# Optimization experiments

Measured on AMD Instinct MI355X. Metric: run time of the kernel, lower is better.

The kernel has to match this reference:

```python
import jax, jax.numpy as jnp
import numpy as np

MARGIN = 0.3


def setup_inputs() -> dict:
    key = jax.random.key(0)
    k1, k2 = jax.random.split(key)
    B, D = 4096, 1024
    z_anchor = jax.random.normal(k1, (B, D), dtype=jnp.float32)
    z_positive = jax.random.normal(k2, (B, D), dtype=jnp.float32)
    return {"z_anchor": z_anchor, "z_positive": z_positive}


def reference(z_anchor, z_positive):
    B = z_anchor.shape[0]
    a = z_anchor / jnp.linalg.norm(z_anchor, axis=1, keepdims=True)
    p = z_positive / jnp.linalg.norm(z_positive, axis=1, keepdims=True)

    pos_dist = 1.0 - jnp.sum(a * p, axis=1)                 # [B]
    neg_dist_mat = 1.0 - jnp.einsum('bd,cd->bc', a, p)      # [B,B]

    offdiag = ~jnp.eye(B, dtype=bool)
    pd = pos_dist[:, None]
    semi_hard = offdiag & (neg_dist_mat > pd) & (neg_dist_mat < pd + MARGIN)

    cnt = jnp.sum(semi_hard, axis=1)                        # [B]
    mean_semi = jnp.sum(jnp.where(semi_hard, neg_dist_mat, 0.0), axis=1) / jnp.maximum(cnt, 1)
    min_offdiag = jnp.min(jnp.where(offdiag, neg_dist_mat, jnp.inf), axis=1)

    neg_dist = jnp.where(cnt > 0, mean_semi, min_offdiag)   # [B]
    loss = jnp.mean(jax.nn.relu(pos_dist - neg_dist + MARGIN))
    return loss
```

## Files before the change

### kernel.cpp

```cpp
#include <hip/hip_runtime.h>
#include <stdint.h>

#define MARGIN 0.3f

typedef __bf16 bf16x8_t __attribute__((ext_vector_type(8)));
typedef float f32x4_t __attribute__((ext_vector_type(4)));

static constexpr int NB = 4096;
static constexpr int ND = 1024;
static constexpr int NKT = ND / 64;
static constexpr int NIT = NKT / 2;

__device__ __forceinline__ unsigned short f2bf(float x) {
  union { float f; unsigned u; } v; v.f = x;
  unsigned r = v.u + 0x7FFFu + ((v.u >> 16) & 1u);
  return (unsigned short)(r >> 16);
}

__device__ __forceinline__ void gload_lds16(const void* g, void* l) {
  __builtin_amdgcn_global_load_lds(
      reinterpret_cast<const __attribute__((address_space(1))) uint32_t*>(
          reinterpret_cast<uintptr_t>(g)),
      reinterpret_cast<__attribute__((address_space(3))) uint32_t*>(
          reinterpret_cast<uintptr_t>(l)),
      16, 0, 0);
}

__global__ __launch_bounds__(256) void norm_kernel(
    const float* __restrict__ za, const float* __restrict__ zp,
    __bf16* __restrict__ Ah, __bf16* __restrict__ Ph,
    float* __restrict__ pos, float* __restrict__ ssum,
    int* __restrict__ scnt, unsigned* __restrict__ smin) {
  const int b = blockIdx.x;
  const int t = threadIdx.x;
  const float4 av = reinterpret_cast<const float4*>(za + (size_t)b * ND)[t];
  const float4 pv = reinterpret_cast<const float4*>(zp + (size_t)b * ND)[t];
  float sa = av.x * av.x + av.y * av.y + av.z * av.z + av.w * av.w;
  float sp = pv.x * pv.x + pv.y * pv.y + pv.z * pv.z + pv.w * pv.w;
  float dp = av.x * pv.x + av.y * pv.y + av.z * pv.z + av.w * pv.w;
#pragma unroll
  for (int off = 1; off < 64; off <<= 1) {
    sa += __shfl_xor(sa, off);
    sp += __shfl_xor(sp, off);
    dp += __shfl_xor(dp, off);
  }
  __shared__ float red[3][4];
  const int wid = t >> 6, lane = t & 63;
  if (lane == 0) { red[0][wid] = sa; red[1][wid] = sp; red[2][wid] = dp; }
  __syncthreads();
  sa = red[0][0] + red[0][1] + red[0][2] + red[0][3];
  sp = red[1][0] + red[1][1] + red[1][2] + red[1][3];
  dp = red[2][0] + red[2][1] + red[2][2] + red[2][3];
  const float rsa = rsqrtf(sa), rsp = rsqrtf(sp);
  if (t == 0) {
    pos[b] = 1.0f - dp * rsa * rsp;
    ssum[b] = 0.0f;
    scnt[b] = 0;
    smin[b] = 0x7F800000u;
  }
  ushort4 oa, op;
  oa.x = f2bf(av.x * rsa); oa.y = f2bf(av.y * rsa);
  oa.z = f2bf(av.z * rsa); oa.w = f2bf(av.w * rsa);
  op.x = f2bf(pv.x * rsp); op.y = f2bf(pv.y * rsp);
  op.z = f2bf(pv.z * rsp); op.w = f2bf(pv.w * rsp);
  reinterpret_cast<ushort4*>(reinterpret_cast<unsigned short*>(Ah) + (size_t)b * ND)[t] = oa;
  reinterpret_cast<ushort4*>(reinterpret_cast<unsigned short*>(Ph) + (size_t)b * ND)[t] = op;
}


#define BAR   __builtin_amdgcn_s_barrier()
#define LGKM0 asm volatile("s_waitcnt lgkmcnt(0)" ::: "memory")
#define VM4   asm volatile("s_waitcnt vmcnt(4)" ::: "memory")
#define VM0   asm volatile("s_waitcnt vmcnt(0)" ::: "memory")
#define PRIO1 __builtin_amdgcn_s_setprio(1)
#define PRIO0 __builtin_amdgcn_s_setprio(0)

#define STAGE_A(buf, half, kt) do { \
    const char* _g = (const char*)Ah + (size_t)(row0 + (half)*128 + srow) * 2048 + (size_t)(kt)*128 + scolb; \
    char* _l = smem + (buf)*32768 + (half)*16384 + w*1024; \
    gload_lds16(_g, _l); \
    gload_lds16(_g + 64*2048, _l + 8192); \
  } while (0)

#define STAGE_B(buf, half, kt) do { \
    const char* _g = (const char*)Ph + (size_t)(col0 + (half)*128 + srow) * 2048 + (size_t)(kt)*128 + scolb; \
    char* _l = smem + 65536 + (buf)*32768 + (half)*16384 + w*1024; \
    gload_lds16(_g, _l); \
    gload_lds16(_g + 64*2048, _l + 8192); \
  } while (0)

#define LD_A(buf, mh) do { _Pragma("unroll") \
    for (int mm = 0; mm < 4; ++mm) { \
      const char* _p = smem + (buf)*32768 + (wr*128 + (mh)*64 + mm*16 + c) * 128; \
      aq[mm][0] = *(const bf16x8_t*)(_p + cswz0); \
      aq[mm][1] = *(const bf16x8_t*)(_p + cswz1); \
    } } while (0)

#define LD_B(buf, nh, dst) do { _Pragma("unroll") \
    for (int nn = 0; nn < 2; ++nn) { \
      const char* _p = smem + 65536 + (buf)*32768 + (wc*64 + (nh)*32 + nn*16 + c) * 128; \
      dst[nn][0] = *(const bf16x8_t*)(_p + cswz0); \
      dst[nn][1] = *(const bf16x8_t*)(_p + cswz1); \
    } } while (0)

#define MFMA_Q(mh, bq, nh) do { _Pragma("unroll") \
    for (int kk = 0; kk < 2; ++kk) { _Pragma("unroll") \
      for (int mm = 0; mm < 4; ++mm) { _Pragma("unroll") \
        for (int nn = 0; nn < 2; ++nn) \
          acc[(mh)*4+mm][(nh)*2+nn] = __builtin_amdgcn_mfma_f32_16x16x32_bf16( \
              aq[mm][kk], bq[nn][kk], acc[(mh)*4+mm][(nh)*2+nn], 0, 0, 0); \
      } } } while (0)

__global__ __launch_bounds__(512, 2) void gemm8_kernel(
    const __bf16* __restrict__ Ah, const __bf16* __restrict__ Ph,
    const float* __restrict__ pos, float* __restrict__ ssum,
    int* __restrict__ scnt, unsigned* __restrict__ smin) {
  extern __shared__ char smem[];
  const int t = threadIdx.x;
  const int lane = t & 63;
  const int w = t >> 6;
  const int wr = w >> 2, wc = w & 3;
  const int c = lane & 15, g = lane >> 4;

  const int wg = blockIdx.x;
  const int swzid = (wg & 7) * 32 + (wg >> 3);
  const int by = swzid >> 4, bx = swzid & 15;
  const int row0 = by * 256, col0 = bx * 256;

  const int srow = w * 8 + (lane >> 3);
  const int scolb = ((lane & 7) << 4) ^ (((lane >> 3) & 7) << 4);
  const int cswz0 = (g * 16) ^ ((c & 7) << 4);
  const int cswz1 = (64 + g * 16) ^ ((c & 7) << 4);

  f32x4_t acc[8][4] = {};
  bf16x8_t aq[4][2], bq0[2][2], bq1[2][2];

  STAGE_B(0, 0, 0); STAGE_B(0, 1, 0);
  STAGE_A(0, 0, 0); STAGE_A(0, 1, 0);
  STAGE_B(1, 0, 1); STAGE_B(1, 1, 1);
  VM4; BAR;

  for (int i = 0; i < NIT; ++i) {
    const int o = 2 * i + 1;
    const bool st = (i < NIT - 1);
    LD_A(0, 0); LD_B(0, 0, bq0);
    STAGE_A(1, 0, o);
    BAR; LGKM0; PRIO1; MFMA_Q(0, bq0, 0); PRIO0; BAR;
    LD_B(0, 1, bq1);
    STAGE_A(1, 1, o);
    BAR; LGKM0; PRIO1; MFMA_Q(0, bq1, 1); PRIO0; BAR;
    LD_A(0, 1);
    if (st) STAGE_B(0, 0, o + 1);
    BAR; LGKM0; PRIO1; MFMA_Q(1, bq0, 0); PRIO0; BAR;
    if (st) STAGE_B(0, 1, o + 1);
    PRIO1; MFMA_Q(1, bq1, 1); PRIO0;
    if (st) { VM4; } else { VM0; }
    BAR;
    LD_A(1, 0); LD_B(1, 0, bq0);
    if (st) STAGE_A(0, 0, o + 1);
    BAR; LGKM0; PRIO1; MFMA_Q(0, bq0, 0); PRIO0; BAR;
    LD_B(1, 1, bq1);
    if (st) STAGE_A(0, 1, o + 1);
    BAR; LGKM0; PRIO1; MFMA_Q(0, bq1, 1); PRIO0; BAR;
    LD_A(1, 1);
    if (st) STAGE_B(1, 0, o + 2);
    BAR; LGKM0; PRIO1; MFMA_Q(1, bq0, 0); PRIO0; BAR;
    if (st) STAGE_B(1, 1, o + 2);
    PRIO1; MFMA_Q(1, bq1, 1); PRIO0;
    if (st) { VM4; } else { VM0; }
    BAR;
  }

#pragma unroll
  for (int m = 0; m < 8; ++m) {
#pragma unroll
    for (int r = 0; r < 4; ++r) {
      const int grow = row0 + wr * 128 + m * 16 + g * 4 + r;
      const float pd = pos[grow];
      float s = 0.0f;
      int ct = 0;
      float mn = 3.0e38f;
#pragma unroll
      for (int n = 0; n < 4; ++n) {
        const int gcol = col0 + wc * 64 + n * 16 + c;
        const float v = 1.0f - acc[m][n][r];
        if (gcol != grow) {
          mn = fminf(mn, v);
          if (v > pd && v < pd + MARGIN) { s += v; ct += 1; }
        }
      }
#pragma unroll
      for (int off = 1; off < 16; off <<= 1) {
        s += __shfl_xor(s, off);
        ct += __shfl_xor(ct, off);
        mn = fminf(mn, __shfl_xor(mn, off));
      }
      if (c == 0) {
        atomicAdd(&ssum[grow], s);
        atomicAdd(&scnt[grow], ct);
        atomicMin(&smin[grow], __float_as_uint(mn));
      }
    }
  }
}

__global__ __launch_bounds__(256) void finalize_kernel(
    const float* __restrict__ pos, const float* __restrict__ ssum,
    const int* __restrict__ scnt, const unsigned* __restrict__ smin,
    float* __restrict__ out) {
  const int t = threadIdx.x;
  float accv = 0.0f;
#pragma unroll
  for (int it = 0; it < NB / 256; ++it) {
    const int rr = t + it * 256;
    const float pd = pos[rr];
    const int ct = scnt[rr];
    const float neg = ct > 0 ? ssum[rr] / (float)ct : __uint_as_float(smin[rr]);
    accv += fmaxf(pd - neg + MARGIN, 0.0f);
  }
#pragma unroll
  for (int off = 1; off < 64; off <<= 1) accv += __shfl_xor(accv, off);
  __shared__ float red[4];
  if ((t & 63) == 0) red[t >> 6] = accv;
  __syncthreads();
  if (t == 0) out[0] = (red[0] + red[1] + red[2] + red[3]) * (1.0f / NB);
}

extern "C" void kernel_launch(void* const* d_in, const int* in_sizes, int n_in,
                              void* d_out, int out_size, void* d_ws, size_t ws_size,
                              hipStream_t stream) {
  const float* za = (const float*)d_in[0];
  const float* zp = (const float*)d_in[1];
  float* out = (float*)d_out;
  char* ws = (char*)d_ws;
  __bf16* Ah = (__bf16*)(ws);
  __bf16* Ph = (__bf16*)(ws + (size_t)NB * ND * 2);
  float* pos = (float*)(ws + (size_t)NB * ND * 4);
  float* ssum = pos + NB;
  int* scnt = (int*)(ssum + NB);
  unsigned* smin = (unsigned*)(scnt + NB);

  (void)hipFuncSetAttribute((const void*)gemm8_kernel,
                            hipFuncAttributeMaxDynamicSharedMemorySize, 131072);

  norm_kernel<<<NB, 256, 0, stream>>>(za, zp, Ah, Ph, pos, ssum, scnt, smin);
  gemm8_kernel<<<256, 512, 131072, stream>>>(Ah, Ph, pos, ssum, scnt, smin);
  finalize_kernel<<<1, 256, 0, stream>>>(pos, ssum, scnt, smin, out);
}
```

Before: 133.8 us.

## Restructure GEMM pipeline with double A register banks and fuse finalize via last-block

```diff
diff --git a/kernel.cpp b/kernel.cpp
--- a/kernel.cpp
+++ b/kernel.cpp
@@ -10,6 +10,7 @@
 static constexpr int ND = 1024;
 static constexpr int NKT = ND / 64;
 static constexpr int NIT = NKT / 2;
+static constexpr int GRID = 256;
 
 __device__ __forceinline__ unsigned short f2bf(float x) {
   union { float f; unsigned u; } v; v.f = x;
@@ -30,7 +31,8 @@
     const float* __restrict__ za, const float* __restrict__ zp,
     __bf16* __restrict__ Ah, __bf16* __restrict__ Ph,
     float* __restrict__ pos, float* __restrict__ ssum,
-    int* __restrict__ scnt, unsigned* __restrict__ smin) {
+    int* __restrict__ scnt, unsigned* __restrict__ smin,
+    int* __restrict__ done) {
   const int b = blockIdx.x;
   const int t = threadIdx.x;
   const float4 av = reinterpret_cast<const float4*>(za + (size_t)b * ND)[t];
@@ -57,6 +59,7 @@
     ssum[b] = 0.0f;
     scnt[b] = 0;
     smin[b] = 0x7F800000u;
+    if (b == 0) *done = 0;
   }
   ushort4 oa, op;
   oa.x = f2bf(av.x * rsa); oa.y = f2bf(av.y * rsa);
@@ -69,9 +72,9 @@
 
 
 #define BAR   __builtin_amdgcn_s_barrier()
-#define LGKM0 asm volatile("s_waitcnt lgkmcnt(0)" ::: "memory")
-#define VM4   asm volatile("s_waitcnt vmcnt(4)" ::: "memory")
-#define VM0   asm volatile("s_waitcnt vmcnt(0)" ::: "memory")
+#define SB0   __builtin_amdgcn_sched_barrier(0)
+#define VM4S  do { asm volatile("s_waitcnt vmcnt(4)" ::: "memory"); SB0; } while (0)
+#define VM0S  do { asm volatile("s_waitcnt vmcnt(0)" ::: "memory"); SB0; } while (0)
 #define PRIO1 __builtin_amdgcn_s_setprio(1)
 #define PRIO0 __builtin_amdgcn_s_setprio(0)
 
@@ -89,32 +92,33 @@
     gload_lds16(_g + 64*2048, _l + 8192); \
   } while (0)
 
-#define LD_A(buf, mh) do { _Pragma("unroll") \
+#define LD_An(buf, mh, bank) do { _Pragma("unroll") \
     for (int mm = 0; mm < 4; ++mm) { \
       const char* _p = smem + (buf)*32768 + (wr*128 + (mh)*64 + mm*16 + c) * 128; \
-      aq[mm][0] = *(const bf16x8_t*)(_p + cswz0); \
-      aq[mm][1] = *(const bf16x8_t*)(_p + cswz1); \
+      bank[mm][0] = *(const bf16x8_t*)(_p + cswz0); \
+      bank[mm][1] = *(const bf16x8_t*)(_p + cswz1); \
     } } while (0)
 
-#define LD_B(buf, nh, dst) do { _Pragma("unroll") \
+#define LD_Bn(buf, nh) do { _Pragma("unroll") \
     for (int nn = 0; nn < 2; ++nn) { \
       const char* _p = smem + 65536 + (buf)*32768 + (wc*64 + (nh)*32 + nn*16 + c) * 128; \
-      dst[nn][0] = *(const bf16x8_t*)(_p + cswz0); \
-      dst[nn][1] = *(const bf16x8_t*)(_p + cswz1); \
+      bq[nn][0] = *(const bf16x8_t*)(_p + cswz0); \
+      bq[nn][1] = *(const bf16x8_t*)(_p + cswz1); \
     } } while (0)
 
-#define MFMA_Q(mh, bq, nh) do { _Pragma("unroll") \
+#define MFMA_Q(mh, nh, ab) do { _Pragma("unroll") \
     for (int kk = 0; kk < 2; ++kk) { _Pragma("unroll") \
       for (int mm = 0; mm < 4; ++mm) { _Pragma("unroll") \
         for (int nn = 0; nn < 2; ++nn) \
           acc[(mh)*4+mm][(nh)*2+nn] = __builtin_amdgcn_mfma_f32_16x16x32_bf16( \
-              aq[mm][kk], bq[nn][kk], acc[(mh)*4+mm][(nh)*2+nn], 0, 0, 0); \
+              ab[mm][kk], bq[nn][kk], acc[(mh)*4+mm][(nh)*2+nn], 0, 0, 0); \
       } } } while (0)
 
 __global__ __launch_bounds__(512, 2) void gemm8_kernel(
     const __bf16* __restrict__ Ah, const __bf16* __restrict__ Ph,
     const float* __restrict__ pos, float* __restrict__ ssum,
-    int* __restrict__ scnt, unsigned* __restrict__ smin) {
+    int* __restrict__ scnt, unsigned* __restrict__ smin,
+    int* __restrict__ done, float* __restrict__ out) {
   extern __shared__ char smem[];
   const int t = threadIdx.x;
   const int lane = t & 63;
@@ -133,42 +137,52 @@
   const int cswz1 = (64 + g * 16) ^ ((c & 7) << 4);
 
   f32x4_t acc[8][4] = {};
-  bf16x8_t aq[4][2], bq0[2][2], bq1[2][2];
-
+  bf16x8_t aqX[4][2], aqY[4][2], bq[2][2];
+
+  STAGE_A(0, 0, 0); STAGE_A(0, 1, 0);
   STAGE_B(0, 0, 0); STAGE_B(0, 1, 0);
-  STAGE_A(0, 0, 0); STAGE_A(0, 1, 0);
-  STAGE_B(1, 0, 1); STAGE_B(1, 1, 1);
-  VM4; BAR;
-
-  for (int i = 0; i < NIT; ++i) {
+  STAGE_A(1, 0, 1); STAGE_A(1, 1, 1);
+  VM4S;
+  BAR;
+  LD_An(0, 0, aqX);
+
+  for (int i = 0; i < NIT - 1; ++i) {
     const int o = 2 * i + 1;
-    const bool st = (i < NIT - 1);
-    LD_A(0, 0); LD_B(0, 0, bq0);
-    STAGE_A(1, 0, o);
-    BAR; LGKM0; PRIO1; MFMA_Q(0, bq0, 0); PRIO0; BAR;
-    LD_B(0, 1, bq1);
-    STAGE_A(1, 1, o);
-    BAR; LGKM0; PRIO1; MFMA_Q(0, bq1, 1); PRIO0; BAR;
-    LD_A(0, 1);
-    if (st) STAGE_B(0, 0, o + 1);
-    BAR; LGKM0; PRIO1; MFMA_Q(1, bq0, 0); PRIO0; BAR;
-    if (st) STAGE_B(0, 1, o + 1);
-    PRIO1; MFMA_Q(1, bq1, 1); PRIO0;
-    if (st) { VM4; } else { VM0; }
-    BAR;
-    LD_A(1, 0); LD_B(1, 0, bq0);
-    if (st) STAGE_A(0, 0, o + 1);
-    BAR; LGKM0; PRIO1; MFMA_Q(0, bq0, 0); PRIO0; BAR;
-    LD_B(1, 1, bq1);
-    if (st) STAGE_A(0, 1, o + 1);
-    BAR; LGKM0; PRIO1; MFMA_Q(0, bq1, 1); PRIO0; BAR;
-    LD_A(1, 1);
-    if (st) STAGE_B(1, 0, o + 2);
-    BAR; LGKM0; PRIO1; MFMA_Q(1, bq0, 0); PRIO0; BAR;
-    if (st) STAGE_B(1, 1, o + 2);
-    PRIO1; MFMA_Q(1, bq1, 1); PRIO0;
-    if (st) { VM4; } else { VM0; }
-    BAR;
+    VM4S; LD_Bn(0, 0); LD_An(0, 1, aqY); STAGE_B(1, 0, o);
+    SB0; BAR; PRIO1; MFMA_Q(0, 0, aqX); PRIO0; BAR;
+    LD_Bn(0, 1); STAGE_B(1, 1, o);
+    SB0; BAR; PRIO1; MFMA_Q(0, 1, aqX); PRIO0; BAR;
+    VM4S; LD_Bn(0, 0); LD_An(1, 0, aqX); STAGE_A(0, 0, o + 1);
+    SB0; BAR; PRIO1; MFMA_Q(1, 0, aqY); PRIO0; BAR;
+    LD_Bn(0, 1); STAGE_A(0, 1, o + 1);
+    SB0; BAR; PRIO1; MFMA_Q(1, 1, aqY); PRIO0; BAR;
+    VM4S; LD_Bn(1, 0); LD_An(1, 1, aqY); STAGE_B(0, 0, o + 1);
+    SB0; BAR; PRIO1; MFMA_Q(0, 0, aqX); PRIO0; BAR;
+    LD_Bn(1, 1); STAGE_B(0, 1, o + 1);
+    SB0; BAR; PRIO1; MFMA_Q(0, 1, aqX); PRIO0; BAR;
+    VM4S; LD_Bn(1, 0); LD_An(0, 0, aqX); STAGE_A(1, 0, o + 2);
+    SB0; BAR; PRIO1; MFMA_Q(1, 0, aqY); PRIO0; BAR;
+    LD_Bn(1, 1); STAGE_A(1, 1, o + 2);
+    SB0; BAR; PRIO1; MFMA_Q(1, 1, aqY); PRIO0; BAR;
+  }
+
+  {
+    VM4S; LD_Bn(0, 0); LD_An(0, 1, aqY); STAGE_B(1, 0, 15);
+    SB0; BAR; PRIO1; MFMA_Q(0, 0, aqX); PRIO0; BAR;
+    LD_Bn(0, 1); STAGE_B(1, 1, 15);
+    SB0; BAR; PRIO1; MFMA_Q(0, 1, aqX); PRIO0; BAR;
+    VM4S; LD_Bn(0, 0); LD_An(1, 0, aqX);
+    SB0; BAR; PRIO1; MFMA_Q(1, 0, aqY); PRIO0; BAR;
+    LD_Bn(0, 1);
+    BAR; PRIO1; MFMA_Q(1, 1, aqY); PRIO0; BAR;
+    VM0S; LD_Bn(1, 0); LD_An(1, 1, aqY);
+    SB0; BAR; PRIO1; MFMA_Q(0, 0, aqX); PRIO0; BAR;
+    LD_Bn(1, 1);
+    BAR; PRIO1; MFMA_Q(0, 1, aqX); PRIO0; BAR;
+    LD_Bn(1, 0);
+    PRIO1; MFMA_Q(1, 0, aqY); PRIO0;
+    LD_Bn(1, 1);
+    PRIO1; MFMA_Q(1, 1, aqY); PRIO0;
   }
 
 #pragma unroll
@@ -202,28 +216,38 @@
       }
     }
   }
-}
-
-__global__ __launch_bounds__(256) void finalize_kernel(
-    const float* __restrict__ pos, const float* __restrict__ ssum,
-    const int* __restrict__ scnt, const unsigned* __restrict__ smin,
-    float* __restrict__ out) {
-  const int t = threadIdx.x;
+
+  __shared__ int lastBlk;
+  __syncthreads();
+  if (t == 0) {
+    __threadfence();
+    lastBlk = (atomicAdd(done, 1) == GRID - 1) ? 1 : 0;
+  }
+  __syncthreads();
+  if (!lastBlk) return;
+
   float accv = 0.0f;
 #pragma unroll
-  for (int it = 0; it < NB / 256; ++it) {
-    const int rr = t + it * 256;
-    const float pd = pos[rr];
-    const int ct = scnt[rr];
-    const float neg = ct > 0 ? ssum[rr] / (float)ct : __uint_as_float(smin[rr]);
+  for (int it = 0; it < NB / 512; ++it) {
+    const int rr = t + it * 512;
+    const float pd = __hip_atomic_load(&pos[rr], __ATOMIC_RELAXED, __HIP_MEMORY_SCOPE_AGENT);
+    const float sm = __hip_atomic_load(&ssum[rr], __ATOMIC_RELAXED, __HIP_MEMORY_SCOPE_AGENT);
+    const int ct = __hip_atomic_load(&scnt[rr], __ATOMIC_RELAXED, __HIP_MEMORY_SCOPE_AGENT);
+    const unsigned mnb = __hip_atomic_load(&smin[rr], __ATOMIC_RELAXED, __HIP_MEMORY_SCOPE_AGENT);
+    const float neg = ct > 0 ? sm / (float)ct : __uint_as_float(mnb);
     accv += fmaxf(pd - neg + MARGIN, 0.0f);
   }
 #pragma unroll
   for (int off = 1; off < 64; off <<= 1) accv += __shfl_xor(accv, off);
-  __shared__ float red[4];
-  if ((t & 63) == 0) red[t >> 6] = accv;
-  __syncthreads();
-  if (t == 0) out[0] = (red[0] + red[1] + red[2] + red[3]) * (1.0f / NB);
+  __shared__ float fred[8];
+  if (lane == 0) fred[w] = accv;
+  __syncthreads();
+  if (t == 0) {
+    float tot = 0.0f;
+#pragma unroll
+    for (int i = 0; i < 8; ++i) tot += fred[i];
+    out[0] = tot * (1.0f / NB);
+  }
 }
 
 extern "C" void kernel_launch(void* const* d_in, const int* in_sizes, int n_in,
@@ -239,11 +263,11 @@
   float* ssum = pos + NB;
   int* scnt = (int*)(ssum + NB);
   unsigned* smin = (unsigned*)(scnt + NB);
+  int* done = (int*)(smin + NB);
 
   (void)hipFuncSetAttribute((const void*)gemm8_kernel,
                             hipFuncAttributeMaxDynamicSharedMemorySize, 131072);
 
-  norm_kernel<<<NB, 256, 0, stream>>>(za, zp, Ah, Ph, pos, ssum, scnt, smin);
-  gemm8_kernel<<<256, 512, 131072, stream>>>(Ah, Ph, pos, ssum, scnt, smin);
-  finalize_kernel<<<1, 256, 0, stream>>>(pos, ssum, scnt, smin, out);
-}
+  norm_kernel<<<NB, 256, 0, stream>>>(za, zp, Ah, Ph, pos, ssum, scnt, smin, done);
+  gemm8_kernel<<<GRID, 512, 131072, stream>>>(Ah, Ph, pos, ssum, scnt, smin, done, out);
+}
```

After: 230.7 us. 1.72x slower.
